# Performance work log

Measured on AMD Instinct MI355X. Metric: run time of the kernel, lower is better.

## Reference

```python
import jax, jax.numpy as jnp
import numpy as np

N = 8192          # number of nodes (dense_shape of the sparse adjacency)
E = 262144        # number of edges (nnz of the sparse tensor), avg degree 32
FLOW_ITERS = 10   # self.flow_iters


def setup_inputs() -> dict:
    key = jax.random.key(0)
    k1, k2, k3, k4 = jax.random.split(key, 4)
    rows = jax.random.randint(k1, (E,), 0, N, dtype=jnp.int32)
    cols = jax.random.randint(k2, (E,), 0, N, dtype=jnp.int32)
    values = jax.random.uniform(k3, (E,), dtype=jnp.float32)      # sparse edge weights (proportions)
    demands = jax.random.normal(k4, (N, 1), dtype=jnp.float32)    # per-node demands
    return {"values": values, "demands": demands, "rows": rows, "cols": cols}


def reference(values, demands, rows, cols):
    d = demands[:, 0]  # [N]

    def step(flow_vals, _):
        # tf.sparse.reduce_sum(flow, axis=0): sum over rows -> per-column inflow [N]
        inflow = jax.ops.segment_sum(flow_vals, cols, num_segments=N)
        # relu(inflow[:, None] - demands) -> per-node adjusted inflow [N]
        adj = jax.nn.relu(inflow - d)
        # sparse * dense with [N,1] broadcast: scale each edge by adj of its row
        return values * adj[rows], None

    flow0 = jnp.zeros_like(values)  # initial empty sparse flow == all-zero values
    flow, _ = jax.lax.scan(step, flow0, None, length=FLOW_ITERS)

    # tf.sparse.to_dense(flow)
    return jnp.zeros((N, N), dtype=values.dtype).at[rows, cols].add(flow)
```

## Files before the change

kernel.cpp:

```cpp
#include <hip/hip_runtime.h>


#define NN 8192
#define EE 262144
#define THREADS 1024
#define SORTB 64
#define EPB (EE / SORTB)
#define NB 256
#define CPB (NN / NB)
#define GROWS 32
#define NBLK 256
#define MAGIC 0x5CA1AB1Eu

typedef unsigned long long u64;

#define LOAD_AU(p)    __hip_atomic_load((p),  __ATOMIC_RELAXED, __HIP_MEMORY_SCOPE_AGENT)
#define STORE_AU(p,v) __hip_atomic_store((p), (v), __ATOMIC_RELAXED, __HIP_MEMORY_SCOPE_AGENT)

#define LBAR() do { asm volatile("s_waitcnt lgkmcnt(0)" ::: "memory"); \
                    __builtin_amdgcn_s_barrier(); \
                    __builtin_amdgcn_sched_barrier(0); } while (0)

union SM {
    struct { unsigned cnt[SORTB * NB]; unsigned hist[NB]; unsigned bst[NB + 1];
             unsigned offs[NB]; } so;
    struct { float acc[CPB]; float dem[CPB]; } c;
    struct { float img[2 * NN]; u64 eL[2048]; } s;
    char pad[90112];
};

__device__ __forceinline__ void flag_barrier_n(unsigned* fl, int idx, int tid, int nblk) {
    if (tid == 0) STORE_AU(&fl[idx], MAGIC);
    asm volatile("" ::: "memory");
    if (tid < 64) {
        for (;;) {
            unsigned f = (tid < nblk) ? LOAD_AU(&fl[tid]) : MAGIC;
            if (__all(f == MAGIC)) break;
            __builtin_amdgcn_s_sleep(2);
        }
    }
    asm volatile("" ::: "memory");
    __syncthreads();
}

__device__ __forceinline__ void flag_barrier_256(unsigned* fl, int idx, int tid) {
    if (tid == 0) STORE_AU(&fl[idx], MAGIC);
    asm volatile("" ::: "memory");
    if (tid < 64) {
        for (;;) {
            unsigned a = LOAD_AU(&fl[tid]);
            unsigned b = LOAD_AU(&fl[tid + 64]);
            unsigned c = LOAD_AU(&fl[tid + 128]);
            unsigned d = LOAD_AU(&fl[tid + 192]);
            if (__all(a == MAGIC && b == MAGIC && c == MAGIC && d == MAGIC)) break;
            __builtin_amdgcn_s_sleep(2);
        }
    }
    asm volatile("" ::: "memory");
    __syncthreads();
}

template <int SLP>
__device__ __forceinline__ void wait_flags_n(unsigned* fl, int tid, int nblk) {
    if (tid < 64) {
        for (;;) {
            unsigned f = (tid < nblk) ? LOAD_AU(&fl[tid]) : MAGIC;
            if (__all(f == MAGIC)) break;
            __builtin_amdgcn_s_sleep(SLP);
        }
    }
    asm volatile("" ::: "memory");
    __syncthreads();
}

__global__ void __launch_bounds__(THREADS) mega(
        const float* __restrict__ values, const float* __restrict__ dem,
        const int* __restrict__ rows, const int* __restrict__ cols,
        u64* __restrict__ se,
        u64* __restrict__ se2,
        float* __restrict__ adjF,
        float* __restrict__ adj9f,
        unsigned* __restrict__ cnt,
        unsigned* __restrict__ cnt2,
        unsigned* __restrict__ bstart,
        unsigned* __restrict__ gstart,
        unsigned* __restrict__ flagsC, unsigned* __restrict__ flagsR,
        unsigned* __restrict__ flagsE, unsigned* __restrict__ flagsR2,
        unsigned* __restrict__ flagsK,
        float* __restrict__ out) {
    __shared__ SM sm;
    __shared__ float a9[GROWS];
    const int bid = blockIdx.x, tid = threadIdx.x;

    if (bid < SORTB) {
        if (tid < NB) sm.so.hist[tid] = 0;
        __syncthreads();
        const int4* c4 = (const int4*)(cols + bid * EPB);
        int4 ca = c4[tid];
        atomicAdd(&sm.so.hist[ca.x >> 5], 1u);  atomicAdd(&sm.so.hist[ca.y >> 5], 1u);
        atomicAdd(&sm.so.hist[ca.z >> 5], 1u);  atomicAdd(&sm.so.hist[ca.w >> 5], 1u);
        __syncthreads();
        if (tid < NB) STORE_AU(&cnt[bid * NB + tid], sm.so.hist[tid]);
        __syncthreads();
        flag_barrier_n(flagsC, bid, tid, SORTB);

        #pragma unroll
        for (int j = 0; j < (SORTB * NB) / THREADS; ++j)
            sm.so.cnt[tid + j * THREADS] = LOAD_AU(&cnt[tid + j * THREADS]);
        __syncthreads();
        if (tid < NB) {
            unsigned t = 0;
            for (int b = 0; b < SORTB; ++b) t += sm.so.cnt[b * NB + tid];
            sm.so.hist[tid] = t;
        }
        __syncthreads();
        if (tid == 0) {
            unsigned run = 0;
            for (int k = 0; k < NB; ++k) { sm.so.bst[k] = run; run += sm.so.hist[k]; }
            sm.so.bst[NB] = run;
        }
        __syncthreads();
        if (tid < NB) {
            unsigned off = sm.so.bst[tid];
            for (int b = 0; b < bid; ++b) off += sm.so.cnt[b * NB + tid];
            sm.so.offs[tid] = off;
        }
        if (bid == 0 && tid <= NB) STORE_AU(&bstart[tid], sm.so.bst[tid]);
        __syncthreads();

        {
            const int4*   r4 = (const int4*)(rows + bid * EPB);
            const float4* v4 = (const float4*)(values + bid * EPB);
            int4 ra = r4[tid];  float4 va = v4[tid];
            #define PUSHC(R, C, V) do {                                        \
                unsigned dst_ = atomicAdd(&sm.so.offs[(C) >> 5], 1u);          \
                u64 w_ = (unsigned)((R) | (((C) & 31) << 13))                  \
                       | ((u64)__float_as_uint(V) << 32);                      \
                STORE_AU(&se[dst_], w_);                                       \
            } while (0)
            PUSHC(ra.x, ca.x, va.x);  PUSHC(ra.y, ca.y, va.y);
            PUSHC(ra.z, ca.z, va.z);  PUSHC(ra.w, ca.w, va.w);
            #undef PUSHC
        }
        __syncthreads();
        flag_barrier_n(flagsE, bid, tid, SORTB);
    } else if (bid < 2 * SORTB) {
        const int b2 = bid - SORTB;
        if (tid < NB) sm.so.hist[tid] = 0;
        __syncthreads();
        const int4* r4 = (const int4*)(rows + b2 * EPB);
        int4 ra = r4[tid];
        atomicAdd(&sm.so.hist[ra.x >> 5], 1u);  atomicAdd(&sm.so.hist[ra.y >> 5], 1u);
        atomicAdd(&sm.so.hist[ra.z >> 5], 1u);  atomicAdd(&sm.so.hist[ra.w >> 5], 1u);
        __syncthreads();
        if (tid < NB) STORE_AU(&cnt2[b2 * NB + tid], sm.so.hist[tid]);
        __syncthreads();
        flag_barrier_n(flagsR, b2, tid, SORTB);

        #pragma unroll
        for (int j = 0; j < (SORTB * NB) / THREADS; ++j)
            sm.so.cnt[tid + j * THREADS] = LOAD_AU(&cnt2[tid + j * THREADS]);
        __syncthreads();
        if (tid < NB) {
            unsigned t = 0;
            for (int b = 0; b < SORTB; ++b) t += sm.so.cnt[b * NB + tid];
            sm.so.hist[tid] = t;
        }
        __syncthreads();
        if (tid == 0) {
            unsigned run = 0;
            for (int k = 0; k < NB; ++k) { sm.so.bst[k] = run; run += sm.so.hist[k]; }
            sm.so.bst[NB] = run;
        }
        __syncthreads();
        if (tid < NB) {
            unsigned off = sm.so.bst[tid];
            for (int b = 0; b < b2; ++b) off += sm.so.cnt[b * NB + tid];
            sm.so.offs[tid] = off;
        }
        if (b2 == 0 && tid <= NB) STORE_AU(&gstart[tid], sm.so.bst[tid]);
        __syncthreads();

        {
            const int4*   c4 = (const int4*)(cols + b2 * EPB);
            const float4* v4 = (const float4*)(values + b2 * EPB);
            int4 ca = c4[tid];  float4 va = v4[tid];
            #define PUSHR(R, C, V) do {                                        \
                unsigned dst_ = atomicAdd(&sm.so.offs[(R) >> 5], 1u);          \
                u64 w_ = (unsigned)((C) | (((R) & 31) << 13))                  \
                       | ((u64)__float_as_uint(V) << 32);                      \
                STORE_AU(&se2[dst_], w_);                                      \
            } while (0)
            PUSHR(ra.x, ca.x, va.x);  PUSHR(ra.y, ca.y, va.y);
            PUSHR(ra.z, ca.z, va.z);  PUSHR(ra.w, ca.w, va.w);
            #undef PUSHR
        }
        __syncthreads();
        if (tid == 0) STORE_AU(&flagsR2[b2], MAGIC);
        asm volatile("" ::: "memory");
        wait_flags_n<4>(flagsE, tid, SORTB);
    } else {
        wait_flags_n<8>(flagsE, tid, SORTB);
    }

    const int bs = (int)LOAD_AU(&bstart[bid]);
    const int be = (int)LOAD_AU(&bstart[bid + 1]);
    const int ne = be - bs;
    u64 e0 = 0, e1 = 0;
    if (tid < ne)           e0 = LOAD_AU(&se[bs + tid]);
    if (THREADS + tid < ne) e1 = LOAD_AU(&se[bs + THREADS + tid]);
    if (tid < CPB) sm.c.dem[tid] = dem[bid * CPB + tid];

    for (int s = 1; s <= 9; ++s) {
        if (tid < CPB) sm.c.acc[tid] = 0.f;
        __syncthreads();

        #define EDGE(W) do {                                                   \
            unsigned m_ = (unsigned)(W);                                       \
            float v_ = __uint_as_float((unsigned)((W) >> 32));                 \
            int r_ = m_ & (NN - 1);                                            \
            float a_ = (s == 1) ? fmaxf(-dem[r_], 0.f)                         \
                                : LOAD_AU(&adjF[(size_t)(s - 1) * NN + r_]);   \
            atomicAdd(&sm.c.acc[(m_ >> 13) & 31], v_ * a_);                    \
        } while (0)
        if (tid < ne)           EDGE(e0);
        if (THREADS + tid < ne) EDGE(e1);
        for (int i = bs + 2 * THREADS + tid; i < be; i += THREADS) {
            u64 w = LOAD_AU(&se[i]);
            EDGE(w);
        }
        #undef EDGE
        __syncthreads();

        if (tid < CPB) {
            float r = fmaxf(sm.c.acc[tid] - sm.c.dem[tid], 0.f);
            if (s < 9) STORE_AU(&adjF[(size_t)s * NN + bid * CPB + tid], r);
            else       STORE_AU(&adj9f[bid * CPB + tid], r);
        }
        __syncthreads();
        flag_barrier_256(flagsK + (s - 1) * NB, bid, tid);
    }
    wait_flags_n<2>(flagsR2, tid, SORTB);

    {
        const int g = bid;
        const unsigned gs = LOAD_AU(&gstart[g]), ge = LOAD_AU(&gstart[g + 1]);
        const unsigned n = ge - gs;
        const unsigned ncp = n < 2048u ? n : 2048u;
        if (tid < GROWS) a9[tid] = LOAD_AU(&adj9f[g * GROWS + tid]);
        __syncthreads();

        for (unsigned i = tid; i < ncp; i += THREADS) {
            u64 w = LOAD_AU(&se2[gs + i]);
            unsigned m = (unsigned)w;
            float v = __uint_as_float((unsigned)(w >> 32));
            sm.s.eL[i] = (u64)m | ((u64)__float_as_uint(v * a9[(m >> 13) & 31]) << 32);
        }
        __syncthreads();

        const float4 z4 = make_float4(0.f, 0.f, 0.f, 0.f);
        for (int r = 0; r < GROWS; ++r) {
            float* im = sm.s.img + (r & 1) * NN;
            ((float4*)im)[tid]        = z4;
            ((float4*)im)[tid + 1024] = z4;
            LBAR();
            for (unsigned i = tid; i < ncp; i += THREADS) {
                u64 w = sm.s.eL[i];
                unsigned m = (unsigned)w;
                if (((m >> 13) & 31) == (unsigned)r)
                    atomicAdd(&im[m & (NN - 1)], __uint_as_float((unsigned)(w >> 32)));
            }
            for (unsigned i = 2048u + tid; i < n; i += THREADS) {
                u64 w = LOAD_AU(&se2[gs + i]);
                unsigned m = (unsigned)w;
                if (((m >> 13) & 31) == (unsigned)r)
                    atomicAdd(&im[m & (NN - 1)],
                              __uint_as_float((unsigned)(w >> 32)) * a9[r]);
            }
            LBAR();
            float4 w0 = ((const float4*)im)[tid];
            float4 w1 = ((const float4*)im)[tid + 1024];
            float4* o4 = (float4*)(out + (size_t)(g * GROWS + r) * NN);
            o4[tid]        = w0;
            o4[tid + 1024] = w1;
        }
    }
}

extern "C" void kernel_launch(void* const* d_in, const int* in_sizes, int n_in,
                              void* d_out, int out_size, void* d_ws, size_t ws_size,
                              hipStream_t stream) {
    const float* values = (const float*)d_in[0];
    const float* dem    = (const float*)d_in[1];
    const int*   rows   = (const int*)d_in[2];
    const int*   cols   = (const int*)d_in[3];
    float* out = (float*)d_out;

    u64*      se      = (u64*)d_ws;
    u64*      se2     = se + (size_t)EE;
    float*    adjF    = (float*)(se2 + (size_t)EE);
    float*    adj9f   = adjF + 9L * NN;
    unsigned* cnt     = (unsigned*)(adj9f + NN);
    unsigned* cnt2    = cnt + SORTB * NB;
    unsigned* bstart  = cnt2 + SORTB * NB;
    unsigned* gstart  = bstart + 320;
    unsigned* flagsC  = gstart + 320;
    unsigned* flagsR  = flagsC + 64;
    unsigned* flagsE  = flagsR + 64;
    unsigned* flagsR2 = flagsE + 64;
    unsigned* flagsK  = flagsR2 + 64;

    mega<<<NBLK, THREADS, 0, stream>>>(
        values, dem, rows, cols, se, se2, adjF, adj9f, cnt, cnt2,
        bstart, gstart, flagsC, flagsR, flagsE, flagsR2, flagsK, out);
}
```

Before: 340.9 us.

## Scatter final edges with global atomics after zero-filling output rows

Result: slower. 356.8 us (+4.6%).

```diff
diff --git a/kernel.cpp b/kernel.cpp
--- a/kernel.cpp
+++ b/kernel.cpp
@@ -17,16 +17,10 @@
 #define LOAD_AU(p)    __hip_atomic_load((p),  __ATOMIC_RELAXED, __HIP_MEMORY_SCOPE_AGENT)
 #define STORE_AU(p,v) __hip_atomic_store((p), (v), __ATOMIC_RELAXED, __HIP_MEMORY_SCOPE_AGENT)
 
-#define LBAR() do { asm volatile("s_waitcnt lgkmcnt(0)" ::: "memory"); \
-                    __builtin_amdgcn_s_barrier(); \
-                    __builtin_amdgcn_sched_barrier(0); } while (0)
-
 union SM {
     struct { unsigned cnt[SORTB * NB]; unsigned hist[NB]; unsigned bst[NB + 1];
              unsigned offs[NB]; } so;
     struct { float acc[CPB]; float dem[CPB]; } c;
-    struct { float img[2 * NN]; u64 eL[2048]; } s;
-    char pad[90112];
 };
 
 __device__ __forceinline__ void flag_barrier_n(unsigned* fl, int idx, int tid, int nblk) {
@@ -245,44 +239,38 @@
     {
         const int g = bid;
         const unsigned gs = LOAD_AU(&gstart[g]), ge = LOAD_AU(&gstart[g + 1]);
-        const unsigned n = ge - gs;
-        const unsigned ncp = n < 2048u ? n : 2048u;
         if (tid < GROWS) a9[tid] = LOAD_AU(&adj9f[g * GROWS + tid]);
         __syncthreads();
 
-        for (unsigned i = tid; i < ncp; i += THREADS) {
-            u64 w = LOAD_AU(&se2[gs + i]);
+        const unsigned i0 = gs + tid, i1 = gs + tid + THREADS;
+        u64 w0 = 0, w1 = 0;
+        if (i0 < ge) w0 = LOAD_AU(&se2[i0]);
+        if (i1 < ge) w1 = LOAD_AU(&se2[i1]);
+
+        float* ob = out + (size_t)g * GROWS * NN;
+        float4* oz = (float4*)ob;
+        const float4 z4 = make_float4(0.f, 0.f, 0.f, 0.f);
+        #pragma unroll 4
+        for (int k = 0; k < (GROWS * NN / 4) / THREADS; ++k)
+            oz[tid + k * THREADS] = z4;
+
+        __syncthreads();
+
+        if (i0 < ge) {
+            unsigned m = (unsigned)w0;
+            float v = __uint_as_float((unsigned)(w0 >> 32)) * a9[(m >> 13) & 31];
+            atomicAdd(&ob[(size_t)((m >> 13) & 31) * NN + (m & (NN - 1))], v);
+        }
+        if (i1 < ge) {
+            unsigned m = (unsigned)w1;
+            float v = __uint_as_float((unsigned)(w1 >> 32)) * a9[(m >> 13) & 31];
+            atomicAdd(&ob[(size_t)((m >> 13) & 31) * NN + (m & (NN - 1))], v);
+        }
+        for (unsigned i = gs + tid + 2 * THREADS; i < ge; i += THREADS) {
+            u64 w = LOAD_AU(&se2[i]);
             unsigned m = (unsigned)w;
-            float v = __uint_as_float((unsigned)(w >> 32));
-            sm.s.eL[i] = (u64)m | ((u64)__float_as_uint(v * a9[(m >> 13) & 31]) << 32);
-        }
-        __syncthreads();
-
-        const float4 z4 = make_float4(0.f, 0.f, 0.f, 0.f);
-        for (int r = 0; r < GROWS; ++r) {
-            float* im = sm.s.img + (r & 1) * NN;
-            ((float4*)im)[tid]        = z4;
-            ((float4*)im)[tid + 1024] = z4;
-            LBAR();
-            for (unsigned i = tid; i < ncp; i += THREADS) {
-                u64 w = sm.s.eL[i];
-                unsigned m = (unsigned)w;
-                if (((m >> 13) & 31) == (unsigned)r)
-                    atomicAdd(&im[m & (NN - 1)], __uint_as_float((unsigned)(w >> 32)));
-            }
-            for (unsigned i = 2048u + tid; i < n; i += THREADS) {
-                u64 w = LOAD_AU(&se2[gs + i]);
-                unsigned m = (unsigned)w;
-                if (((m >> 13) & 31) == (unsigned)r)
-                    atomicAdd(&im[m & (NN - 1)],
-                              __uint_as_float((unsigned)(w >> 32)) * a9[r]);
-            }
-            LBAR();
-            float4 w0 = ((const float4*)im)[tid];
-            float4 w1 = ((const float4*)im)[tid + 1024];
-            float4* o4 = (float4*)(out + (size_t)(g * GROWS + r) * NN);
-            o4[tid]        = w0;
-            o4[tid + 1024] = w1;
+            float v = __uint_as_float((unsigned)(w >> 32)) * a9[(m >> 13) & 31];
+            atomicAdd(&ob[(size_t)((m >> 13) & 31) * NN + (m & (NN - 1))], v);
         }
     }
 }
```
